# Performance work log

Measured on AMD Instinct MI355X. Metric: run time of the kernel, lower is better.

The kernel has to match this reference:

```python
import jax, jax.numpy as jnp
import numpy as np

N_NODES = 30000
N_EDGES = 480000
NODE_DIM = 16
NUM_RADIAL = 8
NUM_ELEMENTS = 120
R_MAX = 5.0
NUM_BLOCKS = 2
N_PATHS = 5  # h0*sh0->0e, h0*sh1->1o, h0*sh2->2e, h1.sh1->0e, h2.sh2->0e


def _sh_basis(u):
    # real spherical harmonics up to l=2, component normalization, on unit vectors u [E,3]
    x, y, z = u[:, 0], u[:, 1], u[:, 2]
    s15 = jnp.sqrt(jnp.asarray(15.0, u.dtype))
    s5 = jnp.sqrt(jnp.asarray(5.0, u.dtype))
    sh1 = jnp.sqrt(jnp.asarray(3.0, u.dtype)) * u                      # [E,3]
    sh2 = jnp.stack([s15 * x * y, s15 * y * z,
                     0.5 * s5 * (3.0 * z * z - 1.0),
                     s15 * x * z, 0.5 * s15 * (x * x - y * y)], -1)    # [E,5]
    return sh1, sh2


def _energy(pos, emb, W_init, Wr, br, W_out, W_read, W1, b1, W2, b2, z, edge_index):
    N = pos.shape[0]
    row, col = edge_index[0], edge_index[1]
    edge_vec = pos[row] - pos[col]                                     # [E,3] gather
    r = jnp.sqrt(jnp.sum(edge_vec * edge_vec, -1) + 1e-12)             # [E]
    n = jnp.arange(1, NUM_RADIAL + 1, dtype=pos.dtype)
    # Bessel radial basis: sqrt(2/rc) * sin(n*pi*r/rc)/r
    radial = jnp.sqrt(2.0 / R_MAX) * jnp.sin(n[None, :] * jnp.pi * r[:, None] / R_MAX) / r[:, None]  # [E,R]
    u = edge_vec / r[:, None]
    sh1, sh2 = _sh_basis(u)

    # initial projection: embedding scalars -> 0e channels; l=1,l=2 start at zero
    h0 = emb[z] @ W_init                                               # [N,C]
    h1 = jnp.zeros((N, NODE_DIM, 3), pos.dtype)
    h2 = jnp.zeros((N, NODE_DIM, 5), pos.dtype)

    for b in range(NUM_BLOCKS):
        w = (radial @ Wr[b] + br[b]).reshape(-1, N_PATHS, NODE_DIM)    # [E,P,C] radial path weights
        h0c, h1c, h2c = h0[col], h1[col], h2[col]
        # scalar messages: h0*sh0 + <h1,sh1> + <h2,sh2>
        m0 = (w[:, 0] * h0c
              + w[:, 3] * jnp.einsum('ecm,em->ec', h1c, sh1)
              + w[:, 4] * jnp.einsum('ecm,em->ec', h2c, sh2))          # [E,C]
        m1 = (w[:, 1] * h0c)[:, :, None] * sh1[:, None, :]             # [E,C,3]
        m2 = (w[:, 2] * h0c)[:, :, None] * sh2[:, None, :]             # [E,C,5]
        a0 = jax.ops.segment_sum(m0, row, num_segments=N)
        a1 = jax.ops.segment_sum(m1, row, num_segments=N)
        a2 = jax.ops.segment_sum(m2, row, num_segments=N)
        h0 = h0 + a0 @ W_out[b, 0]
        h1 = h1 + jnp.einsum('ncm,cd->ndm', a1, W_out[b, 1])
        h2 = h2 + jnp.einsum('ncm,cd->ndm', a2, W_out[b, 2])

    inv = h0 @ W_read                                                  # readout 0e part
    site = jax.nn.silu(inv @ W1 + b1) @ W2 + b2                        # [N,1]
    return jnp.sum(site)


def setup_inputs() -> dict:
    key = jax.random.key(0)
    ks = jax.random.split(key, 12)
    C, R = NODE_DIM, NUM_RADIAL
    s = 1.0 / np.sqrt(C)
    return {
        'pos': jax.random.normal(ks[0], (N_NODES, 3), jnp.float32) * 3.0,
        'z': jax.random.randint(ks[1], (N_NODES,), 0, NUM_ELEMENTS),
        'edge_index': jax.random.randint(ks[2], (2, N_EDGES), 0, N_NODES),
        'emb': jax.random.normal(ks[3], (NUM_ELEMENTS, C), jnp.float32),
        'W_init': jax.random.normal(ks[4], (C, C), jnp.float32) * s,
        'Wr': jax.random.normal(ks[5], (NUM_BLOCKS, R, N_PATHS * C), jnp.float32) / np.sqrt(R),
        'br': jnp.zeros((NUM_BLOCKS, N_PATHS * C), jnp.float32),
        'W_out': jax.random.normal(ks[6], (NUM_BLOCKS, 3, C, C), jnp.float32) * s,
        'W_read': jax.random.normal(ks[7], (C, C), jnp.float32) * s,
        'W1': jax.random.normal(ks[8], (C, C), jnp.float32) * s,
        'b1': jnp.zeros((C,), jnp.float32),
        'W2': jax.random.normal(ks[9], (C, 1), jnp.float32) * s,
        'b2': jnp.zeros((1,), jnp.float32),
    }


def reference(pos, z, edge_index, emb, W_init, Wr, br, W_out, W_read, W1, b1, W2, b2):
    e_fn = lambda p: _energy(p, emb, W_init, Wr, br, W_out, W_read, W1, b1, W2, b2, z, edge_index)
    total, dE_dpos = jax.value_and_grad(e_fn)(pos)
    energy = jnp.reshape(total, (1, 1))
    forces = -dE_dpos
    return energy, forces
```

## Files before the change

### kernel.cpp

```cpp
#include <hip/hip_runtime.h>
#include <math.h>

#ifndef M_PI
#define M_PI 3.14159265358979323846
#endif

static inline int cdiv(int a, int b){ return (a + b - 1) / b; }

#define SQRT3f  1.7320508075688772f
#define SQRT5f  2.23606797749979f
#define SQRT15f 3.872983346207417f
#define KRADf   0.6324555320336759f
#define PI5f    0.6283185307179586f

__device__ __forceinline__ float grp16_sum(float v){
  v += __shfl_xor(v, 1, 64);
  v += __shfl_xor(v, 2, 64);
  v += __shfl_xor(v, 4, 64);
  v += __shfl_xor(v, 8, 64);
  return v;
}
__device__ __forceinline__ float xgrp_sum(float v){
  v += __shfl_xor(v, 16, 64);
  v += __shfl_xor(v, 32, 64);
  return v;
}

__device__ __forceinline__ void sh_from_u(float ux, float uy, float uz,
                                          float* sh1, float* sh2)
{
  sh1[0] = SQRT3f*ux; sh1[1] = SQRT3f*uy; sh1[2] = SQRT3f*uz;
  sh2[0] = SQRT15f*ux*uy;
  sh2[1] = SQRT15f*uy*uz;
  sh2[2] = 0.5f*SQRT5f*(3.f*uz*uz - 1.f);
  sh2[3] = SQRT15f*ux*uz;
  sh2[4] = 0.5f*SQRT15f*(ux*ux - uy*uy);
}

__device__ __forceinline__ void rad_from_sc(float s1, float c1, float inv_r, float* rad)
{
  float tc = 2.f * c1;
  float sprev = 0.f, s = s1;
  float Ki = KRADf * inv_r;
  #pragma unroll
  for (int k = 0; k < 8; k++) {
    rad[k] = Ki * s;
    float sn = tc*s - sprev; sprev = s; s = sn;
  }
}
__device__ __forceinline__ void rad_drad_from_sc(float s1, float c1, float inv_r,
                                                 float* rad, float* draddr)
{
  float tc = 2.f * c1;
  float sprev = 0.f, s = s1, cprev = 1.f, cc = c1;
  float Ki = KRADf * inv_r;
  const float KPI5 = KRADf * PI5f;
  #pragma unroll
  for (int k = 0; k < 8; k++) {
    rad[k] = Ki * s;
    draddr[k] = (KPI5 * (float)(k+1) * cc - rad[k]) * inv_r;
    float sn = tc*s - sprev; sprev = s; s = sn;
    float cn = tc*cc - cprev; cprev = cc; cc = cn;
  }
}

__global__ void k_hist(const int* __restrict__ ei, int E,
                       int* __restrict__ deg_row, int* __restrict__ deg_col)
{
  int e = blockIdx.x * blockDim.x + threadIdx.x;
  if (e >= E) return;
  atomicAdd(&deg_row[ei[e]], 1);
  atomicAdd(&deg_col[ei[E + e]], 1);
}

__global__ void k_alloc(const int* __restrict__ deg_row, const int* __restrict__ deg_col,
                        int* __restrict__ start_row, int* __restrict__ cur_row,
                        int* __restrict__ start_col, int* __restrict__ cur_col,
                        int* __restrict__ cursors, int N)
{
  int idx = blockIdx.x * blockDim.x + threadIdx.x;
  int lane = threadIdx.x & 63;
  #pragma unroll
  for (int which = 0; which < 2; which++) {
    const int* deg = which ? deg_col : deg_row;
    int* start = which ? start_col : start_row;
    int* cur   = which ? cur_col   : cur_row;
    int v = (idx < N) ? deg[idx] : 0;
    int incl = v;
    #pragma unroll
    for (int d = 1; d < 64; d <<= 1) {
      int y = __shfl_up(incl, d, 64);
      if (lane >= d) incl += y;
    }
    int wtot = __shfl(incl, 63, 64);
    int base = 0;
    if (lane == 63) base = atomicAdd(&cursors[which], wtot);
    base = __shfl(base, 63, 64);
    if (idx < N) { int st = base + incl - v; start[idx] = st; cur[idx] = st; }
  }
}

__global__ void k_scatter_geom(const float* __restrict__ pos, const int* __restrict__ ei, int E,
                               int* __restrict__ cur_row, int* __restrict__ cur_col,
                               float4* __restrict__ uR, float2* __restrict__ scR,
                               float4* __restrict__ uC, float2* __restrict__ scC,
                               int* __restrict__ colR, int* __restrict__ cposR,
                               int* __restrict__ rowC, int* __restrict__ rposC)
{
  int e = blockIdx.x * blockDim.x + threadIdx.x;
  if (e >= E) return;
  int row = ei[e], col = ei[E + e];
  int pr = atomicAdd(&cur_row[row], 1);
  int pc = atomicAdd(&cur_col[col], 1);
  colR[pr] = col; cposR[pr] = pc;
  rowC[pc] = row; rposC[pc] = pr;

  float px = pos[row*3+0] - pos[col*3+0];
  float py = pos[row*3+1] - pos[col*3+1];
  float pz = pos[row*3+2] - pos[col*3+2];
  float r2 = px*px + py*py + pz*pz + 1e-12f;
  float r = sqrtf(r2);
  float inv_r = 1.0f / r;
  float ux = px*inv_r, uy = py*inv_r, uz = pz*inv_r;
  float s1, c1;
  sincosf(r * PI5f, &s1, &c1);
  float4 u4 = make_float4(ux, uy, uz, inv_r);
  float2 sc = make_float2(s1, c1);
  uR[pr] = u4; scR[pr] = sc;
  uC[pc] = u4; scC[pc] = sc;
}

__global__ void k_node_init(const float* __restrict__ emb, const int* __restrict__ z,
                            const float* __restrict__ W_init, float* __restrict__ h0, int N)
{
  __shared__ float sW[256];
  if (threadIdx.x < 256) sW[threadIdx.x] = W_init[threadIdx.x];
  __syncthreads();
  int n = blockIdx.x * blockDim.x + threadIdx.x;
  if (n >= N) return;
  const float* e = emb + z[n]*16;
  float ev[16];
  #pragma unroll
  for (int k = 0; k < 16; k++) ev[k] = e[k];
  #pragma unroll
  for (int c = 0; c < 16; c++) {
    float s = 0.f;
    #pragma unroll
    for (int k = 0; k < 16; k++) s += ev[k] * sW[k*16+c];
    h0[n*16+c] = s;
  }
}

__global__ void k_fwd_b0(const float* __restrict__ Wr, const float* __restrict__ br,
                         const float* __restrict__ h0_in,
                         const float4* __restrict__ uR, const float2* __restrict__ scR,
                         const int* __restrict__ colR,
                         const int* __restrict__ start_row, const int* __restrict__ deg_row,
                         float* __restrict__ a0, float* __restrict__ a1, float* __restrict__ a2,
                         int N)
{
  int n = (blockIdx.x * blockDim.x + threadIdx.x) >> 6;
  int lane = threadIdx.x & 63;
  int g = lane >> 4, c = lane & 15;
  if (n >= N) return;
  float wr0[8], wr1[8], wr2[8];
  #pragma unroll
  for (int k = 0; k < 8; k++) {
    wr0[k] = Wr[k*80 + c];
    wr1[k] = Wr[k*80 + 16 + c];
    wr2[k] = Wr[k*80 + 32 + c];
  }
  float b0v = br[c], b1v = br[16 + c], b2v = br[32 + c];

  float acc0 = 0.f, acc1[3] = {0.f,0.f,0.f}, acc2[5] = {0.f,0.f,0.f,0.f,0.f};

  int i0 = start_row[n] + g, i1 = start_row[n] + deg_row[n];
  float4 Un = {0,0,0,0}; float2 SCn = {0,0};
  float h0n = 0.f;
  if (i0 < i1) {
    Un = uR[i0]; SCn = scR[i0];
    h0n = h0_in[colR[i0]*16 + c];
  }
  for (int i = i0; i < i1; i += 4) {
    float4 U = Un; float2 SC = SCn;
    float h0c = h0n;
    if (i+4 < i1) {
      Un = uR[i+4]; SCn = scR[i+4];
      h0n = h0_in[colR[i+4]*16 + c];
    }
    float rad[8];
    rad_from_sc(SC.x, SC.y, U.w, rad);
    float sh1[3], sh2[5];
    sh_from_u(U.x, U.y, U.z, sh1, sh2);
    float w0 = b0v, w1 = b1v, w2 = b2v;
    #pragma unroll
    for (int k = 0; k < 8; k++) {
      w0 += rad[k]*wr0[k]; w1 += rad[k]*wr1[k]; w2 += rad[k]*wr2[k];
    }
    acc0 += w0*h0c;
    float wh1 = w1*h0c, wh2 = w2*h0c;
    #pragma unroll
    for (int m = 0; m < 3; m++) acc1[m] += wh1*sh1[m];
    #pragma unroll
    for (int m = 0; m < 5; m++) acc2[m] += wh2*sh2[m];
  }
  acc0 = xgrp_sum(acc0);
  #pragma unroll
  for (int m = 0; m < 3; m++) acc1[m] = xgrp_sum(acc1[m]);
  #pragma unroll
  for (int m = 0; m < 5; m++) acc2[m] = xgrp_sum(acc2[m]);
  if (g == 0) {
    a0[n*16 + c] = acc0;
    #pragma unroll
    for (int m = 0; m < 3; m++) a1[n*48 + c*3 + m] = acc1[m];
    #pragma unroll
    for (int m = 0; m < 5; m++) a2[n*80 + c*5 + m] = acc2[m];
  }
}

__global__ void k_fwd_b1(const float* __restrict__ Wr, const float* __restrict__ br,
                         const float* __restrict__ h0_in, const float* __restrict__ h1_in,
                         const float* __restrict__ h2_in,
                         const float4* __restrict__ uR, const float2* __restrict__ scR,
                         const int* __restrict__ colR,
                         const int* __restrict__ start_row, const int* __restrict__ deg_row,
                         float* __restrict__ a0, int N)
{
  int n = (blockIdx.x * blockDim.x + threadIdx.x) >> 6;
  int lane = threadIdx.x & 63;
  int g = lane >> 4, c = lane & 15;
  if (n >= N) return;
  float wr0[8], wr3[8], wr4[8];
  #pragma unroll
  for (int k = 0; k < 8; k++) {
    wr0[k] = Wr[k*80 + c];
    wr3[k] = Wr[k*80 + 48 + c];
    wr4[k] = Wr[k*80 + 64 + c];
  }
  float b0v = br[c], b3v = br[48 + c], b4v = br[64 + c];

  float acc0 = 0.f;
  int i0 = start_row[n] + g, i1 = start_row[n] + deg_row[n];
  float4 Un = {0,0,0,0}; float2 SCn = {0,0};
  float h0n = 0.f, h1n[3] = {0,0,0}, h2n[5] = {0,0,0,0,0};
  if (i0 < i1) {
    int col = colR[i0];
    Un = uR[i0]; SCn = scR[i0];
    h0n = h0_in[col*16 + c];
    #pragma unroll
    for (int m = 0; m < 3; m++) h1n[m] = h1_in[col*48 + c*3 + m];
    #pragma unroll
    for (int m = 0; m < 5; m++) h2n[m] = h2_in[col*80 + c*5 + m];
  }
  for (int i = i0; i < i1; i += 4) {
    float4 U = Un; float2 SC = SCn;
    float h0c = h0n;
    float h1c[3], h2c[5];
    #pragma unroll
    for (int m = 0; m < 3; m++) h1c[m] = h1n[m];
    #pragma unroll
    for (int m = 0; m < 5; m++) h2c[m] = h2n[m];
    if (i+4 < i1) {
      int col = colR[i+4];
      Un = uR[i+4]; SCn = scR[i+4];
      h0n = h0_in[col*16 + c];
      #pragma unroll
      for (int m = 0; m < 3; m++) h1n[m] = h1_in[col*48 + c*3 + m];
      #pragma unroll
      for (int m = 0; m < 5; m++) h2n[m] = h2_in[col*80 + c*5 + m];
    }
    float rad[8];
    rad_from_sc(SC.x, SC.y, U.w, rad);
    float sh1[3], sh2[5];
    sh_from_u(U.x, U.y, U.z, sh1, sh2);
    float w0 = b0v, w3 = b3v, w4 = b4v;
    #pragma unroll
    for (int k = 0; k < 8; k++) {
      w0 += rad[k]*wr0[k]; w3 += rad[k]*wr3[k]; w4 += rad[k]*wr4[k];
    }
    float S1 = 0.f, S2 = 0.f;
    #pragma unroll
    for (int m = 0; m < 3; m++) S1 += h1c[m]*sh1[m];
    #pragma unroll
    for (int m = 0; m < 5; m++) S2 += h2c[m]*sh2[m];
    acc0 += w0*h0c + w3*S1 + w4*S2;
  }
  acc0 = xgrp_sum(acc0);
  if (g == 0) a0[n*16 + c] = acc0;
}

__global__ void k_node_update(const float* __restrict__ h0_in,
                              const float* __restrict__ a0, const float* __restrict__ a1,
                              const float* __restrict__ a2,
                              const float* __restrict__ U,
                              float* __restrict__ h0_out, float* __restrict__ h1_out,
                              float* __restrict__ h2_out, int N)
{
  int idx = blockIdx.x * blockDim.x + threadIdx.x;
  int n = idx >> 4, d = idx & 15;
  if (n >= N) return;
  const float* U0 = U;
  const float* U1 = U + 256;
  const float* U2 = U + 512;
  float s = h0_in[n*16 + d];
  #pragma unroll
  for (int c = 0; c < 16; c++) s += a0[n*16 + c] * U0[c*16 + d];
  h0_out[n*16 + d] = s;
  float v1[3] = {0.f, 0.f, 0.f};
  #pragma unroll
  for (int c = 0; c < 16; c++) {
    float u = U1[c*16 + d];
    #pragma unroll
    for (int m = 0; m < 3; m++) v1[m] += a1[n*48 + c*3 + m] * u;
  }
  #pragma unroll
  for (int m = 0; m < 3; m++) h1_out[n*48 + d*3 + m] = v1[m];
  float v2[5] = {0.f, 0.f, 0.f, 0.f, 0.f};
  #pragma unroll
  for (int c = 0; c < 16; c++) {
    float u = U2[c*16 + d];
    #pragma unroll
    for (int m = 0; m < 5; m++) v2[m] += a2[n*80 + c*5 + m] * u;
  }
  #pragma unroll
  for (int m = 0; m < 5; m++) h2_out[n*80 + d*5 + m] = v2[m];
}

__global__ void __launch_bounds__(256, 1)
k_readout_bwd(const float* __restrict__ h0s1, const float* __restrict__ a0in,
              const float* __restrict__ W_read,
              const float* __restrict__ W1, const float* __restrict__ b1,
              const float* __restrict__ W2, const float* __restrict__ b2,
              const float* __restrict__ U0b1,
              float* __restrict__ g0, float* __restrict__ ga0,
              float* __restrict__ partials, int N)
{
  __shared__ float sWr[256], sW1[256], sU[256], sb1[16], sW2[16], sb2;
  __shared__ float swave[4];
  {
    int t = threadIdx.x;
    if (t < 256) { sWr[t] = W_read[t]; sW1[t] = W1[t]; sU[t] = U0b1[t]; }
// ... 74 lines not shown
  #pragma unroll
  for (int off = 32; off; off >>= 1) s += __shfl_down(s, off, 64);
  __shared__ float sw[2];
  if ((t & 63) == 0) sw[t >> 6] = s;
  __syncthreads();
  if (t == 0) energy[0] = sw[0] + sw[1];
}

__global__ void k_ga(const float* __restrict__ g0, const float* __restrict__ g1,
                     const float* __restrict__ g2, const float* __restrict__ U,
                     float* __restrict__ ga0, float* __restrict__ ga1, float* __restrict__ ga2,
                     int N)
{
  int idx = blockIdx.x * blockDim.x + threadIdx.x;
  int n = idx >> 4, c = idx & 15;
  if (n >= N) return;
  const float* U0 = U;
  const float* U1 = U + 256;
  const float* U2 = U + 512;
  float s = 0.f;
  #pragma unroll
  for (int d = 0; d < 16; d++) s += g0[n*16 + d] * U0[c*16 + d];
  ga0[n*16 + c] = s;
  float v1[3] = {0.f, 0.f, 0.f};
  #pragma unroll
  for (int d = 0; d < 16; d++) {
    float u = U1[c*16 + d];
    #pragma unroll
    for (int m = 0; m < 3; m++) v1[m] += g1[n*48 + d*3 + m] * u;
  }
  #pragma unroll
  for (int m = 0; m < 3; m++) ga1[n*48 + c*3 + m] = v1[m];
  float v2[5] = {0.f, 0.f, 0.f, 0.f, 0.f};
  #pragma unroll
  for (int d = 0; d < 16; d++) {
    float u = U2[c*16 + d];
    #pragma unroll
    for (int m = 0; m < 5; m++) v2[m] += g2[n*80 + d*5 + m] * u;
  }
  #pragma unroll
  for (int m = 0; m < 5; m++) ga2[n*80 + c*5 + m] = v2[m];
}

__global__ void k_bwd_b1_col(const float* __restrict__ Wr, const float* __restrict__ br,
                             const float* __restrict__ h0_in, const float* __restrict__ h1_in,
                             const float* __restrict__ h2_in,
                             const float* __restrict__ ga0,
                             const float4* __restrict__ uC, const float2* __restrict__ scC,
                             const int* __restrict__ rowC,
                             const int* __restrict__ start_col, const int* __restrict__ deg_col,
                             float* __restrict__ g0, float* __restrict__ g1, float* __restrict__ g2,
                             float* __restrict__ dv_col, int N)
{
  int n = (blockIdx.x * blockDim.x + threadIdx.x) >> 6;
  int lane = threadIdx.x & 63;
  int g = lane >> 4, c = lane & 15;
  if (n >= N) return;
  float wr0[8], wr3[8], wr4[8];
  #pragma unroll
  for (int k = 0; k < 8; k++) {
    wr0[k] = Wr[k*80 + c];
    wr3[k] = Wr[k*80 + 48 + c];
    wr4[k] = Wr[k*80 + 64 + c];
  }
  float b0v = br[c], b3v = br[48 + c], b4v = br[64 + c];

  float h0c = h0_in[n*16 + c];
  float h1c[3], h2c[5];
  #pragma unroll
  for (int m = 0; m < 3; m++) h1c[m] = h1_in[n*48 + c*3 + m];
  #pragma unroll
  for (int m = 0; m < 5; m++) h2c[m] = h2_in[n*80 + c*5 + m];

  float accg0 = 0.f, accg1[3] = {0.f,0.f,0.f}, accg2[5] = {0.f,0.f,0.f,0.f,0.f};

  int i0 = start_col[n] + g, i1 = start_col[n] + deg_col[n];
  float4 Un = {0,0,0,0}; float2 SCn = {0,0};
  float dm0n = 0.f;
  if (i0 < i1) {
    Un = uC[i0]; SCn = scC[i0];
    dm0n = ga0[rowC[i0]*16 + c];
  }
  for (int i = i0; i < i1; i += 4) {
    float4 U = Un; float2 SC = SCn;
    float dm0 = dm0n;
    if (i+4 < i1) {
      Un = uC[i+4]; SCn = scC[i+4];
      dm0n = ga0[rowC[i+4]*16 + c];
    }
    float rad[8], draddr[8];
    rad_drad_from_sc(SC.x, SC.y, U.w, rad, draddr);
    float ux = U.x, uy = U.y, uz = U.z, inv_r = U.w;
    float sh1[3], sh2[5];
    sh_from_u(ux, uy, uz, sh1, sh2);

    float w0 = b0v, w3 = b3v, w4 = b4v;
    #pragma unroll
    for (int k = 0; k < 8; k++) {
      w0 += rad[k]*wr0[k]; w3 += rad[k]*wr3[k]; w4 += rad[k]*wr4[k];
    }

    float S1 = 0.f, S2 = 0.f;
    #pragma unroll
    for (int m = 0; m < 3; m++) S1 += h1c[m]*sh1[m];
    #pragma unroll
    for (int m = 0; m < 5; m++) S2 += h2c[m]*sh2[m];

    float dw0 = dm0 * h0c;
    float dw3 = dm0 * S1;
    float dw4 = dm0 * S2;
    float t3 = dm0 * w3, t4 = dm0 * w4;

    accg0 += dm0 * w0;
    #pragma unroll
    for (int m = 0; m < 3; m++) accg1[m] += t3 * sh1[m];
    #pragma unroll
    for (int m = 0; m < 5; m++) accg2[m] += t4 * sh2[m];

    float q1x = t3*h1c[0], q1y = t3*h1c[1], q1z = t3*h1c[2];
    float q0 = t4*h2c[0], q1 = t4*h2c[1], q2 = t4*h2c[2], q3 = t4*h2c[3], q4 = t4*h2c[4];
    float gr = 0.f;
    #pragma unroll
    for (int k = 0; k < 8; k++)
      gr += (dw0*wr0[k] + dw3*wr3[k] + dw4*wr4[k]) * draddr[k];
    float gux = SQRT3f*q1x + SQRT15f*(uy*q0 + uz*q3 + ux*q4);
    float guy = SQRT3f*q1y + SQRT15f*(ux*q0 + uz*q1 - uy*q4);
    float guz = SQRT3f*q1z + SQRT15f*uy*q1 + 3.f*SQRT5f*uz*q2 + SQRT15f*ux*q3;

    gr  = grp16_sum(gr);
    gux = grp16_sum(gux);
    guy = grp16_sum(guy);
    guz = grp16_sum(guz);

    if (c == 0) {
      float gdotu = gux*ux + guy*uy + guz*uz;
      dv_col[i*3+0] = gr*ux + (gux - gdotu*ux)*inv_r;
      dv_col[i*3+1] = gr*uy + (guy - gdotu*uy)*inv_r;
      dv_col[i*3+2] = gr*uz + (guz - gdotu*uz)*inv_r;
    }
  }
  accg0 = xgrp_sum(accg0);
  #pragma unroll
  for (int m = 0; m < 3; m++) accg1[m] = xgrp_sum(accg1[m]);
  #pragma unroll
  for (int m = 0; m < 5; m++) accg2[m] = xgrp_sum(accg2[m]);
  if (g == 0) {
    g0[n*16 + c] += accg0;
    #pragma unroll
    for (int m = 0; m < 3; m++) g1[n*48 + c*3 + m] = accg1[m];
    #pragma unroll
    for (int m = 0; m < 5; m++) g2[n*80 + c*5 + m] = accg2[m];
  }
}

__global__ void k_bwd_b0_row(const float* __restrict__ Wr, const float* __restrict__ br,
                             const float* __restrict__ h0_in,
                             const float* __restrict__ ga0, const float* __restrict__ ga1,
                             const float* __restrict__ ga2,
                             const float4* __restrict__ uR, const float2* __restrict__ scR,
                             const int* __restrict__ colR,
                             const int* __restrict__ start_row, const int* __restrict__ deg_row,
                             float* __restrict__ dv_row, int N)
{
  int n = (blockIdx.x * blockDim.x + threadIdx.x) >> 6;
  int lane = threadIdx.x & 63;
  int g = lane >> 4, c = lane & 15;
  if (n >= N) return;
  float wr0[8], wr1[8], wr2[8];
  #pragma unroll
  for (int k = 0; k < 8; k++) {
    wr0[k] = Wr[k*80 + c];
    wr1[k] = Wr[k*80 + 16 + c];
    wr2[k] = Wr[k*80 + 32 + c];
  }
  float b1v = br[16 + c], b2v = br[32 + c];

  float dm0 = ga0[n*16 + c];
  float dm1[3], dm2[5];
  #pragma unroll
  for (int m = 0; m < 3; m++) dm1[m] = ga1[n*48 + c*3 + m];
  #pragma unroll
  for (int m = 0; m < 5; m++) dm2[m] = ga2[n*80 + c*5 + m];

  int i0 = start_row[n] + g, i1 = start_row[n] + deg_row[n];
  float4 Un = {0,0,0,0}; float2 SCn = {0,0};
  float h0n = 0.f;
  if (i0 < i1) {
    Un = uR[i0]; SCn = scR[i0];
    h0n = h0_in[colR[i0]*16 + c];
  }
  for (int i = i0; i < i1; i += 4) {
    float4 U = Un; float2 SC = SCn;
    float h0c = h0n;
    if (i+4 < i1) {
      Un = uR[i+4]; SCn = scR[i+4];
      h0n = h0_in[colR[i+4]*16 + c];
    }
    float rad[8], draddr[8];
    rad_drad_from_sc(SC.x, SC.y, U.w, rad, draddr);
    float ux = U.x, uy = U.y, uz = U.z, inv_r = U.w;
    float sh1[3], sh2[5];
    sh_from_u(ux, uy, uz, sh1, sh2);

    float w1 = b1v, w2v = b2v;
    #pragma unroll
    for (int k = 0; k < 8; k++) { w1 += rad[k]*wr1[k]; w2v += rad[k]*wr2[k]; }

    float T1 = 0.f, T2 = 0.f;
    #pragma unroll
    for (int m = 0; m < 3; m++) T1 += dm1[m]*sh1[m];
    #pragma unroll
    for (int m = 0; m < 5; m++) T2 += dm2[m]*sh2[m];

    float dw0 = dm0 * h0c;
    float dw1 = h0c * T1;
    float dw2 = h0c * T2;

    float w1h = w1*h0c, w2h = w2v*h0c;
    float q1x = dm1[0]*w1h, q1y = dm1[1]*w1h, q1z = dm1[2]*w1h;
    float q0 = dm2[0]*w2h, q1 = dm2[1]*w2h, q2 = dm2[2]*w2h, q3 = dm2[3]*w2h, q4 = dm2[4]*w2h;

    float gr = 0.f;
    #pragma unroll
    for (int k = 0; k < 8; k++)
      gr += (dw0*wr0[k] + dw1*wr1[k] + dw2*wr2[k]) * draddr[k];
    float gux = SQRT3f*q1x + SQRT15f*(uy*q0 + uz*q3 + ux*q4);
    float guy = SQRT3f*q1y + SQRT15f*(ux*q0 + uz*q1 - uy*q4);
    float guz = SQRT3f*q1z + SQRT15f*uy*q1 + 3.f*SQRT5f*uz*q2 + SQRT15f*ux*q3;

    gr  = grp16_sum(gr);
    gux = grp16_sum(gux);
    guy = grp16_sum(guy);
    guz = grp16_sum(guz);

    if (c == 0) {
      float gdotu = gux*ux + guy*uy + guz*uz;
      dv_row[i*3+0] = gr*ux + (gux - gdotu*ux)*inv_r;
      dv_row[i*3+1] = gr*uy + (guy - gdotu*uy)*inv_r;
      dv_row[i*3+2] = gr*uz + (guz - gdotu*uz)*inv_r;
    }
  }
}

__global__ void k_force(const int* __restrict__ start_row, const int* __restrict__ deg_row,
                        const int* __restrict__ cposR,
                        const int* __restrict__ start_col, const int* __restrict__ deg_col,
                        const int* __restrict__ rposC,
                        const float* __restrict__ dv_col, const float* __restrict__ dv_row,
                        float* __restrict__ force, int N)
{
  int n = blockIdx.x * blockDim.x + threadIdx.x;
  if (n >= N) return;
  float fx = 0.f, fy = 0.f, fz = 0.f;
  int c0 = start_col[n], c1 = c0 + deg_col[n];
  for (int i = c0; i < c1; i++) {
    int rp = rposC[i];
    fx += dv_col[i*3+0] + dv_row[rp*3+0];
    fy += dv_col[i*3+1] + dv_row[rp*3+1];
    fz += dv_col[i*3+2] + dv_row[rp*3+2];
  }
  int r0 = start_row[n], r1 = r0 + deg_row[n];
  for (int i = r0; i < r1; i++) {
    int cp = cposR[i];
    fx -= dv_row[i*3+0] + dv_col[cp*3+0];
    fy -= dv_row[i*3+1] + dv_col[cp*3+1];
    fz -= dv_row[i*3+2] + dv_col[cp*3+2];
  }
  force[n*3+0] = fx; force[n*3+1] = fy; force[n*3+2] = fz;
}

extern "C" void kernel_launch(void* const* d_in, const int* in_sizes, int n_in,
                              void* d_out, int out_size, void* d_ws, size_t ws_size,
                              hipStream_t stream)
{
  const float* pos    = (const float*)d_in[0];
  const int*   z      = (const int*)  d_in[1];
  const int*   ei     = (const int*)  d_in[2];
  const float* emb    = (const float*)d_in[3];
  const float* W_init = (const float*)d_in[4];
  const float* Wr     = (const float*)d_in[5];
  const float* br     = (const float*)d_in[6];
  const float* W_out  = (const float*)d_in[7];
  const float* W_read = (const float*)d_in[8];
  const float* W1     = (const float*)d_in[9];
  const float* b1     = (const float*)d_in[10];
  const float* W2     = (const float*)d_in[11];
  const float* b2     = (const float*)d_in[12];

  const int N = in_sizes[0] / 3;
  const int E = in_sizes[2] / 2;

  const int BLK = 256;
  const int NPB = BLK / 64;
  const int NB_READOUT = cdiv(N, BLK);

  float* f = (float*)d_ws;
  float4* uR  = (float4*)f; f += (size_t)E*4;
  float4* uC  = (float4*)f; f += (size_t)E*4;
  float2* scR = (float2*)f; f += (size_t)E*2;
  float2* scC = (float2*)f; f += (size_t)E*2;
  float* h0_s0 = f; f += (size_t)N*16;
  float* h0_s1 = f; f += (size_t)N*16;
  float* h1_s1 = f; f += (size_t)N*48;
  float* h2_s1 = f; f += (size_t)N*80;
  float* a0    = f; f += (size_t)N*16;
  float* a1    = f; f += (size_t)N*48;
  float* a2    = f; f += (size_t)N*80;
  float* ga0b1 = f; f += (size_t)N*16;
  float* g0    = f; f += (size_t)N*16;
  float* g1    = f; f += (size_t)N*48;
  float* g2    = f; f += (size_t)N*80;
  float* dv_c  = f; f += (size_t)E*3;
  float* dv_r  = f; f += (size_t)E*3;
  float* partials = f; f += (size_t)NB_READOUT;
  int* ip = (int*)f;
  int* cursors   = ip; ip += 2;
  int* deg_row   = ip; ip += N;
  int* deg_col   = ip; ip += N;
  int* start_row = ip; ip += N;
  int* start_col = ip; ip += N;
  int* cur_row   = ip; ip += N;
  int* cur_col   = ip; ip += N;
  int* colR      = ip; ip += E;
  int* cposR     = ip; ip += E;
  int* rowC      = ip; ip += E;
  int* rposC     = ip; ip += E;

  float* out    = (float*)d_out;
  float* energy = out;
  float* force  = out + 1;

  (void)hipMemsetAsync(cursors, 0, (size_t)(2 + 2*N) * sizeof(int), stream);

  k_hist<<<cdiv(E, BLK), BLK, 0, stream>>>(ei, E, deg_row, deg_col);
  k_alloc<<<cdiv(N, BLK), BLK, 0, stream>>>(deg_row, deg_col, start_row, cur_row,
                                            start_col, cur_col, cursors, N);
  k_scatter_geom<<<cdiv(E, BLK), BLK, 0, stream>>>(pos, ei, E, cur_row, cur_col,
                                                   uR, scR, uC, scC,
                                                   colR, cposR, rowC, rposC);

  k_node_init<<<cdiv(N, BLK), BLK, 0, stream>>>(emb, z, W_init, h0_s0, N);

  k_fwd_b0<<<cdiv(N, NPB), BLK, 0, stream>>>(Wr, br, h0_s0, uR, scR, colR,
                                             start_row, deg_row, a0, a1, a2, N);
  k_node_update<<<cdiv(N*16, BLK), BLK, 0, stream>>>(h0_s0, a0, a1, a2,
                                                     W_out, h0_s1, h1_s1, h2_s1, N);

  k_fwd_b1<<<cdiv(N, NPB), BLK, 0, stream>>>(Wr + 640, br + 80,
                                             h0_s1, h1_s1, h2_s1, uR, scR, colR,
                                             start_row, deg_row, a0, N);

  k_readout_bwd<<<NB_READOUT, BLK, 0, stream>>>(h0_s1, a0, W_read, W1, b1, W2, b2,
                                                W_out + 768, g0, ga0b1, partials, N);
  k_energy<<<1, 128, 0, stream>>>(partials, NB_READOUT, energy);

  k_bwd_b1_col<<<cdiv(N, NPB), BLK, 0, stream>>>(Wr + 640, br + 80,
                                                 h0_s1, h1_s1, h2_s1, ga0b1,
                                                 uC, scC, rowC, start_col, deg_col,
                                                 g0, g1, g2, dv_c, N);

  k_ga<<<cdiv(N*16, BLK), BLK, 0, stream>>>(g0, g1, g2, W_out, a0, a1, a2, N);
  k_bwd_b0_row<<<cdiv(N, NPB), BLK, 0, stream>>>(Wr, br, h0_s0,
                                                 a0, a1, a2, uR, scR, colR,
                                                 start_row, deg_row, dv_r, N);

  k_force<<<cdiv(N, BLK), BLK, 0, stream>>>(start_row, deg_row, cposR,
                                            start_col, deg_col, rposC,
                                            dv_c, dv_r, force, N);
}
```

Before: 497.3 us.

## Use persistent grid-stride edge kernels, fuse radial recurrence, parallelize force gather

The four per-node edge kernels now run as persistent grid-stride loops with a fixed grid of 2048 blocks. This amortizes the per-warp loading of the radial weight registers across many nodes. The radial basis and its derivative are computed inline within the weight accumulation, and the derivative dot product is folded into two scalar accumulators, which avoids holding rad/draddr arrays and lowers register pressure. The force kernel uses 16 lanes per node with a shuffle reduction instead of one thread walking all edges. The fixed grid size may limit load balance or occupancy on skewed degree distributions.

New measurement: 473.4 us. 4.8% less time.

```diff
diff --git a/kernel.cpp b/kernel.cpp
--- a/kernel.cpp
+++ b/kernel.cpp
@@ -12,6 +12,8 @@
 #define SQRT15f 3.872983346207417f
 #define KRADf   0.6324555320336759f
 #define PI5f    0.6283185307179586f
+#define KPI5f   (KRADf * PI5f)
+
 
 __device__ __forceinline__ float grp16_sum(float v){
   v += __shfl_xor(v, 1, 64);
@@ -37,32 +39,6 @@
   sh2[4] = 0.5f*SQRT15f*(ux*ux - uy*uy);
 }
 
-__device__ __forceinline__ void rad_from_sc(float s1, float c1, float inv_r, float* rad)
-{
-  float tc = 2.f * c1;
-  float sprev = 0.f, s = s1;
-  float Ki = KRADf * inv_r;
-  #pragma unroll
-  for (int k = 0; k < 8; k++) {
-    rad[k] = Ki * s;
-    float sn = tc*s - sprev; sprev = s; s = sn;
-  }
-}
-__device__ __forceinline__ void rad_drad_from_sc(float s1, float c1, float inv_r,
-                                                 float* rad, float* draddr)
-{
-  float tc = 2.f * c1;
-  float sprev = 0.f, s = s1, cprev = 1.f, cc = c1;
-  float Ki = KRADf * inv_r;
-  const float KPI5 = KRADf * PI5f;
-  #pragma unroll
-  for (int k = 0; k < 8; k++) {
-    rad[k] = Ki * s;
-    draddr[k] = (KPI5 * (float)(k+1) * cc - rad[k]) * inv_r;
-    float sn = tc*s - sprev; sprev = s; s = sn;
-    float cn = tc*cc - cprev; cprev = cc; cc = cn;
-  }
-}
 
 __global__ void k_hist(const int* __restrict__ ei, int E,
                        int* __restrict__ deg_row, int* __restrict__ deg_col)
@@ -159,10 +135,10 @@
                          float* __restrict__ a0, float* __restrict__ a1, float* __restrict__ a2,
                          int N)
 {
-  int n = (blockIdx.x * blockDim.x + threadIdx.x) >> 6;
+  int wid = (blockIdx.x * blockDim.x + threadIdx.x) >> 6;
+  int nw  = (gridDim.x * blockDim.x) >> 6;
   int lane = threadIdx.x & 63;
   int g = lane >> 4, c = lane & 15;
-  if (n >= N) return;
   float wr0[8], wr1[8], wr2[8];
   #pragma unroll
   for (int k = 0; k < 8; k++) {
@@ -172,49 +148,54 @@
   }
   float b0v = br[c], b1v = br[16 + c], b2v = br[32 + c];
 
-  float acc0 = 0.f, acc1[3] = {0.f,0.f,0.f}, acc2[5] = {0.f,0.f,0.f,0.f,0.f};
-
-  int i0 = start_row[n] + g, i1 = start_row[n] + deg_row[n];
-  float4 Un = {0,0,0,0}; float2 SCn = {0,0};
-  float h0n = 0.f;
-  if (i0 < i1) {
-    Un = uR[i0]; SCn = scR[i0];
-    h0n = h0_in[colR[i0]*16 + c];
-  }
-  for (int i = i0; i < i1; i += 4) {
-    float4 U = Un; float2 SC = SCn;
-    float h0c = h0n;
-    if (i+4 < i1) {
-      Un = uR[i+4]; SCn = scR[i+4];
-      h0n = h0_in[colR[i+4]*16 + c];
-    }
-    float rad[8];
-    rad_from_sc(SC.x, SC.y, U.w, rad);
-    float sh1[3], sh2[5];
-    sh_from_u(U.x, U.y, U.z, sh1, sh2);
-    float w0 = b0v, w1 = b1v, w2 = b2v;
-    #pragma unroll
-    for (int k = 0; k < 8; k++) {
-      w0 += rad[k]*wr0[k]; w1 += rad[k]*wr1[k]; w2 += rad[k]*wr2[k];
-    }
-    acc0 += w0*h0c;
-    float wh1 = w1*h0c, wh2 = w2*h0c;
-    #pragma unroll
-    for (int m = 0; m < 3; m++) acc1[m] += wh1*sh1[m];
-    #pragma unroll
-    for (int m = 0; m < 5; m++) acc2[m] += wh2*sh2[m];
-  }
-  acc0 = xgrp_sum(acc0);
-  #pragma unroll
-  for (int m = 0; m < 3; m++) acc1[m] = xgrp_sum(acc1[m]);
-  #pragma unroll
-  for (int m = 0; m < 5; m++) acc2[m] = xgrp_sum(acc2[m]);
-  if (g == 0) {
-    a0[n*16 + c] = acc0;
-    #pragma unroll
-    for (int m = 0; m < 3; m++) a1[n*48 + c*3 + m] = acc1[m];
-    #pragma unroll
-    for (int m = 0; m < 5; m++) a2[n*80 + c*5 + m] = acc2[m];
+  for (int n = wid; n < N; n += nw) {
+    float acc0 = 0.f, acc1[3] = {0.f,0.f,0.f}, acc2[5] = {0.f,0.f,0.f,0.f,0.f};
+
+    int i0 = start_row[n] + g, i1 = start_row[n] + deg_row[n];
+    float4 Un = {0,0,0,0}; float2 SCn = {0,0};
+    float h0n = 0.f;
+    if (i0 < i1) {
+      Un = uR[i0]; SCn = scR[i0];
+      h0n = h0_in[colR[i0]*16 + c];
+    }
+    for (int i = i0; i < i1; i += 4) {
+      float4 U = Un; float2 SC = SCn;
+      float h0c = h0n;
+      if (i+4 < i1) {
+        Un = uR[i+4]; SCn = scR[i+4];
+        h0n = h0_in[colR[i+4]*16 + c];
+      }
+      float Ki = KRADf * U.w;
+      float tc = 2.f * SC.y;
+      float sprev = 0.f, s = SC.x;
+      float w0 = b0v, w1 = b1v, w2 = b2v;
+      #pragma unroll
+      for (int k = 0; k < 8; k++) {
+        float rad = Ki * s;
+        w0 += rad*wr0[k]; w1 += rad*wr1[k]; w2 += rad*wr2[k];
+        float sn = tc*s - sprev; sprev = s; s = sn;
+      }
+      float sh1[3], sh2[5];
+      sh_from_u(U.x, U.y, U.z, sh1, sh2);
+      acc0 += w0*h0c;
+      float wh1 = w1*h0c, wh2 = w2*h0c;
+      #pragma unroll
+      for (int m = 0; m < 3; m++) acc1[m] += wh1*sh1[m];
+      #pragma unroll
+      for (int m = 0; m < 5; m++) acc2[m] += wh2*sh2[m];
+    }
+    acc0 = xgrp_sum(acc0);
+    #pragma unroll
+    for (int m = 0; m < 3; m++) acc1[m] = xgrp_sum(acc1[m]);
+    #pragma unroll
+    for (int m = 0; m < 5; m++) acc2[m] = xgrp_sum(acc2[m]);
+    if (g == 0) {
+      a0[n*16 + c] = acc0;
+      #pragma unroll
+      for (int m = 0; m < 3; m++) a1[n*48 + c*3 + m] = acc1[m];
+      #pragma unroll
+      for (int m = 0; m < 5; m++) a2[n*80 + c*5 + m] = acc2[m];
+    }
   }
 }
 
@@ -226,10 +207,10 @@
                          const int* __restrict__ start_row, const int* __restrict__ deg_row,
                          float* __restrict__ a0, int N)
 {
-  int n = (blockIdx.x * blockDim.x + threadIdx.x) >> 6;
+  int wid = (blockIdx.x * blockDim.x + threadIdx.x) >> 6;
+  int nw  = (gridDim.x * blockDim.x) >> 6;
   int lane = threadIdx.x & 63;
   int g = lane >> 4, c = lane & 15;
-  if (n >= N) return;
   float wr0[8], wr3[8], wr4[8];
   #pragma unroll
   for (int k = 0; k < 8; k++) {
@@ -239,54 +220,59 @@
   }
   float b0v = br[c], b3v = br[48 + c], b4v = br[64 + c];
 
-  float acc0 = 0.f;
-  int i0 = start_row[n] + g, i1 = start_row[n] + deg_row[n];
-  float4 Un = {0,0,0,0}; float2 SCn = {0,0};
-  float h0n = 0.f, h1n[3] = {0,0,0}, h2n[5] = {0,0,0,0,0};
-  if (i0 < i1) {
-    int col = colR[i0];
-    Un = uR[i0]; SCn = scR[i0];
-    h0n = h0_in[col*16 + c];
-    #pragma unroll
-    for (int m = 0; m < 3; m++) h1n[m] = h1_in[col*48 + c*3 + m];
-    #pragma unroll
-    for (int m = 0; m < 5; m++) h2n[m] = h2_in[col*80 + c*5 + m];
-  }
-  for (int i = i0; i < i1; i += 4) {
-    float4 U = Un; float2 SC = SCn;
-    float h0c = h0n;
-    float h1c[3], h2c[5];
-    #pragma unroll
-    for (int m = 0; m < 3; m++) h1c[m] = h1n[m];
-    #pragma unroll
-    for (int m = 0; m < 5; m++) h2c[m] = h2n[m];
-    if (i+4 < i1) {
-      int col = colR[i+4];
-      Un = uR[i+4]; SCn = scR[i+4];
+  for (int n = wid; n < N; n += nw) {
+    float acc0 = 0.f;
+    int i0 = start_row[n] + g, i1 = start_row[n] + deg_row[n];
+    float4 Un = {0,0,0,0}; float2 SCn = {0,0};
+    float h0n = 0.f, h1n[3] = {0,0,0}, h2n[5] = {0,0,0,0,0};
+    if (i0 < i1) {
+      int col = colR[i0];
+      Un = uR[i0]; SCn = scR[i0];
       h0n = h0_in[col*16 + c];
       #pragma unroll
       for (int m = 0; m < 3; m++) h1n[m] = h1_in[col*48 + c*3 + m];
       #pragma unroll
       for (int m = 0; m < 5; m++) h2n[m] = h2_in[col*80 + c*5 + m];
     }
-    float rad[8];
-    rad_from_sc(SC.x, SC.y, U.w, rad);
-    float sh1[3], sh2[5];
-    sh_from_u(U.x, U.y, U.z, sh1, sh2);
-    float w0 = b0v, w3 = b3v, w4 = b4v;
-    #pragma unroll
-    for (int k = 0; k < 8; k++) {
-      w0 += rad[k]*wr0[k]; w3 += rad[k]*wr3[k]; w4 += rad[k]*wr4[k];
-    }
-    float S1 = 0.f, S2 = 0.f;
-    #pragma unroll
-    for (int m = 0; m < 3; m++) S1 += h1c[m]*sh1[m];
-    #pragma unroll
-    for (int m = 0; m < 5; m++) S2 += h2c[m]*sh2[m];
-    acc0 += w0*h0c + w3*S1 + w4*S2;
-  }
-  acc0 = xgrp_sum(acc0);
-  if (g == 0) a0[n*16 + c] = acc0;
+    for (int i = i0; i < i1; i += 4) {
+      float4 U = Un; float2 SC = SCn;
+      float h0c = h0n;
+      float h1c[3], h2c[5];
+      #pragma unroll
+      for (int m = 0; m < 3; m++) h1c[m] = h1n[m];
+      #pragma unroll
+      for (int m = 0; m < 5; m++) h2c[m] = h2n[m];
+      if (i+4 < i1) {
+        int col = colR[i+4];
+        Un = uR[i+4]; SCn = scR[i+4];
+        h0n = h0_in[col*16 + c];
+        #pragma unroll
+        for (int m = 0; m < 3; m++) h1n[m] = h1_in[col*48 + c*3 + m];
+        #pragma unroll
+        for (int m = 0; m < 5; m++) h2n[m] = h2_in[col*80 + c*5 + m];
+      }
+      float Ki = KRADf * U.w;
+      float tc = 2.f * SC.y;
+      float sprev = 0.f, s = SC.x;
+      float w0 = b0v, w3 = b3v, w4 = b4v;
+      #pragma unroll
+      for (int k = 0; k < 8; k++) {
+        float rad = Ki * s;
+        w0 += rad*wr0[k]; w3 += rad*wr3[k]; w4 += rad*wr4[k];
+        float sn = tc*s - sprev; sprev = s; s = sn;
+      }
+      float sh1[3], sh2[5];
+      sh_from_u(U.x, U.y, U.z, sh1, sh2);
+      float S1 = 0.f, S2 = 0.f;
+      #pragma unroll
+      for (int m = 0; m < 3; m++) S1 += h1c[m]*sh1[m];
+      #pragma unroll
+      for (int m = 0; m < 5; m++) S2 += h2c[m]*sh2[m];
+      acc0 += w0*h0c + w3*S1 + w4*S2;
+    }
+    acc0 = xgrp_sum(acc0);
+    if (g == 0) a0[n*16 + c] = acc0;
+  }
 }
 
 __global__ void k_node_update(const float* __restrict__ h0_in,
@@ -467,10 +453,10 @@
                              float* __restrict__ g0, float* __restrict__ g1, float* __restrict__ g2,
                              float* __restrict__ dv_col, int N)
 {
-  int n = (blockIdx.x * blockDim.x + threadIdx.x) >> 6;
+  int wid = (blockIdx.x * blockDim.x + threadIdx.x) >> 6;
+  int nw  = (gridDim.x * blockDim.x) >> 6;
   int lane = threadIdx.x & 63;
   int g = lane >> 4, c = lane & 15;
-  if (n >= N) return;
   float wr0[8], wr3[8], wr4[8];
   #pragma unroll
   for (int k = 0; k < 8; k++) {
@@ -480,91 +466,98 @@
   }
   float b0v = br[c], b3v = br[48 + c], b4v = br[64 + c];
 
-  float h0c = h0_in[n*16 + c];
-  float h1c[3], h2c[5];
-  #pragma unroll
-  for (int m = 0; m < 3; m++) h1c[m] = h1_in[n*48 + c*3 + m];
-  #pragma unroll
-  for (int m = 0; m < 5; m++) h2c[m] = h2_in[n*80 + c*5 + m];
-
-  float accg0 = 0.f, accg1[3] = {0.f,0.f,0.f}, accg2[5] = {0.f,0.f,0.f,0.f,0.f};
-
-  int i0 = start_col[n] + g, i1 = start_col[n] + deg_col[n];
-  float4 Un = {0,0,0,0}; float2 SCn = {0,0};
-  float dm0n = 0.f;
-  if (i0 < i1) {
-    Un = uC[i0]; SCn = scC[i0];
-    dm0n = ga0[rowC[i0]*16 + c];
-  }
-  for (int i = i0; i < i1; i += 4) {
-    float4 U = Un; float2 SC = SCn;
-    float dm0 = dm0n;
-    if (i+4 < i1) {
-      Un = uC[i+4]; SCn = scC[i+4];
-      dm0n = ga0[rowC[i+4]*16 + c];
-    }
-    float rad[8], draddr[8];
-    rad_drad_from_sc(SC.x, SC.y, U.w, rad, draddr);
-    float ux = U.x, uy = U.y, uz = U.z, inv_r = U.w;
-    float sh1[3], sh2[5];
-    sh_from_u(ux, uy, uz, sh1, sh2);
-
-    float w0 = b0v, w3 = b3v, w4 = b4v;
-    #pragma unroll
-    for (int k = 0; k < 8; k++) {
-      w0 += rad[k]*wr0[k]; w3 += rad[k]*wr3[k]; w4 += rad[k]*wr4[k];
-    }
-
-    float S1 = 0.f, S2 = 0.f;
-    #pragma unroll
-    for (int m = 0; m < 3; m++) S1 += h1c[m]*sh1[m];
-    #pragma unroll
-    for (int m = 0; m < 5; m++) S2 += h2c[m]*sh2[m];
-
-    float dw0 = dm0 * h0c;
-    float dw3 = dm0 * S1;
-    float dw4 = dm0 * S2;
-    float t3 = dm0 * w3, t4 = dm0 * w4;
-
-    accg0 += dm0 * w0;
-    #pragma unroll
-    for (int m = 0; m < 3; m++) accg1[m] += t3 * sh1[m];
-    #pragma unroll
-    for (int m = 0; m < 5; m++) accg2[m] += t4 * sh2[m];
-
-    float q1x = t3*h1c[0], q1y = t3*h1c[1], q1z = t3*h1c[2];
-    float q0 = t4*h2c[0], q1 = t4*h2c[1], q2 = t4*h2c[2], q3 = t4*h2c[3], q4 = t4*h2c[4];
-    float gr = 0.f;
-    #pragma unroll
-    for (int k = 0; k < 8; k++)
-      gr += (dw0*wr0[k] + dw3*wr3[k] + dw4*wr4[k]) * draddr[k];
-    float gux = SQRT3f*q1x + SQRT15f*(uy*q0 + uz*q3 + ux*q4);
-    float guy = SQRT3f*q1y + SQRT15f*(ux*q0 + uz*q1 - uy*q4);
-    float guz = SQRT3f*q1z + SQRT15f*uy*q1 + 3.f*SQRT5f*uz*q2 + SQRT15f*ux*q3;
-
-    gr  = grp16_sum(gr);
-    gux = grp16_sum(gux);
-    guy = grp16_sum(guy);
-    guz = grp16_sum(guz);
-
-    if (c == 0) {
-      float gdotu = gux*ux + guy*uy + guz*uz;
-      dv_col[i*3+0] = gr*ux + (gux - gdotu*ux)*inv_r;
-      dv_col[i*3+1] = gr*uy + (guy - gdotu*uy)*inv_r;
-      dv_col[i*3+2] = gr*uz + (guz - gdotu*uz)*inv_r;
-    }
-  }
-  accg0 = xgrp_sum(accg0);
-  #pragma unroll
-  for (int m = 0; m < 3; m++) accg1[m] = xgrp_sum(accg1[m]);
-  #pragma unroll
-  for (int m = 0; m < 5; m++) accg2[m] = xgrp_sum(accg2[m]);
-  if (g == 0) {
-    g0[n*16 + c] += accg0;
-    #pragma unroll
-    for (int m = 0; m < 3; m++) g1[n*48 + c*3 + m] = accg1[m];
-    #pragma unroll
-    for (int m = 0; m < 5; m++) g2[n*80 + c*5 + m] = accg2[m];
+  for (int n = wid; n < N; n += nw) {
+    float h0c = h0_in[n*16 + c];
+    float h1c[3], h2c[5];
+    #pragma unroll
+    for (int m = 0; m < 3; m++) h1c[m] = h1_in[n*48 + c*3 + m];
+    #pragma unroll
+    for (int m = 0; m < 5; m++) h2c[m] = h2_in[n*80 + c*5 + m];
+
+    float accg0 = 0.f, accg1[3] = {0.f,0.f,0.f}, accg2[5] = {0.f,0.f,0.f,0.f,0.f};
+
+    int i0 = start_col[n] + g, i1 = start_col[n] + deg_col[n];
+    float4 Un = {0,0,0,0}; float2 SCn = {0,0};
+    float dm0n = 0.f;
+    if (i0 < i1) {
+      Un = uC[i0]; SCn = scC[i0];
+      dm0n = ga0[rowC[i0]*16 + c];
+    }
+    for (int i = i0; i < i1; i += 4) {
+      float4 U = Un; float2 SC = SCn;
+      float dm0 = dm0n;
+      if (i+4 < i1) {
+        Un = uC[i+4]; SCn = scC[i+4];
+        dm0n = ga0[rowC[i+4]*16 + c];
+      }
+      float ux = U.x, uy = U.y, uz = U.z, inv_r = U.w;
+      float sh1[3], sh2[5];
+      sh_from_u(ux, uy, uz, sh1, sh2);
+
+      float S1 = 0.f, S2 = 0.f;
+      #pragma unroll
+      for (int m = 0; m < 3; m++) S1 += h1c[m]*sh1[m];
+      #pragma unroll
+      for (int m = 0; m < 5; m++) S2 += h2c[m]*sh2[m];
+
+      float dw0 = dm0 * h0c;
+      float dw3 = dm0 * S1;
+      float dw4 = dm0 * S2;
+
+      float Ki = KRADf * inv_r;
+      float tc = 2.f * SC.y;
+      float sprev = 0.f, s = SC.x, cprev = 1.f, cc = SC.y;
+      float w0 = b0v, w3 = b3v, w4 = b4v;
+      float P = 0.f, Q = 0.f;
+      #pragma unroll
+      for (int k = 0; k < 8; k++) {
+        float rad = Ki * s;
+        w0 += rad*wr0[k]; w3 += rad*wr3[k]; w4 += rad*wr4[k];
+        float t = dw0*wr0[k] + dw3*wr3[k] + dw4*wr4[k];
+        P = fmaf(t*cc, (float)(k+1), P);
+        Q = fmaf(t, rad, Q);
+        float sn = tc*s - sprev; sprev = s; s = sn;
+        float cn = tc*cc - cprev; cprev = cc; cc = cn;
+      }
+
+      float t3 = dm0 * w3, t4 = dm0 * w4;
+      accg0 += dm0 * w0;
+      #pragma unroll
+      for (int m = 0; m < 3; m++) accg1[m] += t3 * sh1[m];
+      #pragma unroll
+      for (int m = 0; m < 5; m++) accg2[m] += t4 * sh2[m];
+
+      float q1x = t3*h1c[0], q1y = t3*h1c[1], q1z = t3*h1c[2];
+      float q0 = t4*h2c[0], q1 = t4*h2c[1], q2 = t4*h2c[2], q3 = t4*h2c[3], q4 = t4*h2c[4];
+      float gr = (KPI5f*P - Q) * inv_r;
+      float gux = SQRT3f*q1x + SQRT15f*(uy*q0 + uz*q3 + ux*q4);
+      float guy = SQRT3f*q1y + SQRT15f*(ux*q0 + uz*q1 - uy*q4);
+      float guz = SQRT3f*q1z + SQRT15f*uy*q1 + 3.f*SQRT5f*uz*q2 + SQRT15f*ux*q3;
+
+      gr  = grp16_sum(gr);
+      gux = grp16_sum(gux);
+      guy = grp16_sum(guy);
+      guz = grp16_sum(guz);
+
+      if (c == 0) {
+        float gdotu = gux*ux + guy*uy + guz*uz;
+        dv_col[i*3+0] = gr*ux + (gux - gdotu*ux)*inv_r;
+        dv_col[i*3+1] = gr*uy + (guy - gdotu*uy)*inv_r;
+        dv_col[i*3+2] = gr*uz + (guz - gdotu*uz)*inv_r;
+      }
+    }
+    accg0 = xgrp_sum(accg0);
+    #pragma unroll
+    for (int m = 0; m < 3; m++) accg1[m] = xgrp_sum(accg1[m]);
+    #pragma unroll
+    for (int m = 0; m < 5; m++) accg2[m] = xgrp_sum(accg2[m]);
+    if (g == 0) {
+      g0[n*16 + c] += accg0;
+      #pragma unroll
+      for (int m = 0; m < 3; m++) g1[n*48 + c*3 + m] = accg1[m];
+      #pragma unroll
+      for (int m = 0; m < 5; m++) g2[n*80 + c*5 + m] = accg2[m];
+    }
   }
 }
 
@@ -577,10 +570,10 @@
                              const int* __restrict__ start_row, const int* __restrict__ deg_row,
                              float* __restrict__ dv_row, int N)
 {
-  int n = (blockIdx.x * blockDim.x + threadIdx.x) >> 6;
+  int wid = (blockIdx.x * blockDim.x + threadIdx.x) >> 6;
+  int nw  = (gridDim.x * blockDim.x) >> 6;
   int lane = threadIdx.x & 63;
   int g = lane >> 4, c = lane & 15;
-  if (n >= N) return;
   float wr0[8], wr1[8], wr2[8];
   #pragma unroll
   for (int k = 0; k < 8; k++) {
@@ -590,69 +583,78 @@
   }
   float b1v = br[16 + c], b2v = br[32 + c];
 
-  float dm0 = ga0[n*16 + c];
-  float dm1[3], dm2[5];
-  #pragma unroll
-  for (int m = 0; m < 3; m++) dm1[m] = ga1[n*48 + c*3 + m];
-  #pragma unroll
-  for (int m = 0; m < 5; m++) dm2[m] = ga2[n*80 + c*5 + m];
-
-  int i0 = start_row[n] + g, i1 = start_row[n] + deg_row[n];
-  float4 Un = {0,0,0,0}; float2 SCn = {0,0};
-  float h0n = 0.f;
-  if (i0 < i1) {
-    Un = uR[i0]; SCn = scR[i0];
-    h0n = h0_in[colR[i0]*16 + c];
-  }
-  for (int i = i0; i < i1; i += 4) {
-    float4 U = Un; float2 SC = SCn;
-    float h0c = h0n;
-    if (i+4 < i1) {
-      Un = uR[i+4]; SCn = scR[i+4];
-      h0n = h0_in[colR[i+4]*16 + c];
-    }
-    float rad[8], draddr[8];
-    rad_drad_from_sc(SC.x, SC.y, U.w, rad, draddr);
-    float ux = U.x, uy = U.y, uz = U.z, inv_r = U.w;
-    float sh1[3], sh2[5];
-    sh_from_u(ux, uy, uz, sh1, sh2);
-
-    float w1 = b1v, w2v = b2v;
-    #pragma unroll
-    for (int k = 0; k < 8; k++) { w1 += rad[k]*wr1[k]; w2v += rad[k]*wr2[k]; }
-
-    float T1 = 0.f, T2 = 0.f;
-    #pragma unroll
-    for (int m = 0; m < 3; m++) T1 += dm1[m]*sh1[m];
-    #pragma unroll
-    for (int m = 0; m < 5; m++) T2 += dm2[m]*sh2[m];
-
-    float dw0 = dm0 * h0c;
-    float dw1 = h0c * T1;
-    float dw2 = h0c * T2;
-
-    float w1h = w1*h0c, w2h = w2v*h0c;
-    float q1x = dm1[0]*w1h, q1y = dm1[1]*w1h, q1z = dm1[2]*w1h;
-    float q0 = dm2[0]*w2h, q1 = dm2[1]*w2h, q2 = dm2[2]*w2h, q3 = dm2[3]*w2h, q4 = dm2[4]*w2h;
-
-    float gr = 0.f;
-    #pragma unroll
-    for (int k = 0; k < 8; k++)
-      gr += (dw0*wr0[k] + dw1*wr1[k] + dw2*wr2[k]) * draddr[k];
-    float gux = SQRT3f*q1x + SQRT15f*(uy*q0 + uz*q3 + ux*q4);
-    float guy = SQRT3f*q1y + SQRT15f*(ux*q0 + uz*q1 - uy*q4);
-    float guz = SQRT3f*q1z + SQRT15f*uy*q1 + 3.f*SQRT5f*uz*q2 + SQRT15f*ux*q3;
-
-    gr  = grp16_sum(gr);
-    gux = grp16_sum(gux);
-    guy = grp16_sum(guy);
-    guz = grp16_sum(guz);
-
-    if (c == 0) {
-      float gdotu = gux*ux + guy*uy + guz*uz;
-      dv_row[i*3+0] = gr*ux + (gux - gdotu*ux)*inv_r;
-      dv_row[i*3+1] = gr*uy + (guy - gdotu*uy)*inv_r;
-      dv_row[i*3+2] = gr*uz + (guz - gdotu*uz)*inv_r;
+  for (int n = wid; n < N; n += nw) {
+    float dm0 = ga0[n*16 + c];
+    float dm1[3], dm2[5];
+    #pragma unroll
+    for (int m = 0; m < 3; m++) dm1[m] = ga1[n*48 + c*3 + m];
+    #pragma unroll
+    for (int m = 0; m < 5; m++) dm2[m] = ga2[n*80 + c*5 + m];
+
+    int i0 = start_row[n] + g, i1 = start_row[n] + deg_row[n];
+    float4 Un = {0,0,0,0}; float2 SCn = {0,0};
+    float h0n = 0.f;
+    if (i0 < i1) {
+      Un = uR[i0]; SCn = scR[i0];
+      h0n = h0_in[colR[i0]*16 + c];
+    }
+    for (int i = i0; i < i1; i += 4) {
+      float4 U = Un; float2 SC = SCn;
+      float h0c = h0n;
+      if (i+4 < i1) {
+        Un = uR[i+4]; SCn = scR[i+4];
+        h0n = h0_in[colR[i+4]*16 + c];
+      }
+      float ux = U.x, uy = U.y, uz = U.z, inv_r = U.w;
+      float sh1[3], sh2[5];
+      sh_from_u(ux, uy, uz, sh1, sh2);
+
+      float T1 = 0.f, T2 = 0.f;
+      #pragma unroll
+      for (int m = 0; m < 3; m++) T1 += dm1[m]*sh1[m];
+      #pragma unroll
+      for (int m = 0; m < 5; m++) T2 += dm2[m]*sh2[m];
+
+      float dw0 = dm0 * h0c;
+      float dw1 = h0c * T1;
+      float dw2 = h0c * T2;
+
+      float Ki = KRADf * inv_r;
+      float tc = 2.f * SC.y;
+      float sprev = 0.f, s = SC.x, cprev = 1.f, cc = SC.y;
+      float w1 = b1v, w2v = b2v;
+      float P = 0.f, Q = 0.f;
+      #pragma unroll
+      for (int k = 0; k < 8; k++) {
+        float rad = Ki * s;
+        w1 += rad*wr1[k]; w2v += rad*wr2[k];
+        float t = dw0*wr0[k] + dw1*wr1[k] + dw2*wr2[k];
+        P = fmaf(t*cc, (float)(k+1), P);
+        Q = fmaf(t, rad, Q);
+        float sn = tc*s - sprev; sprev = s; s = sn;
+        float cn = tc*cc - cprev; cprev = cc; cc = cn;
+      }
+
+      float w1h = w1*h0c, w2h = w2v*h0c;
+      float q1x = dm1[0]*w1h, q1y = dm1[1]*w1h, q1z = dm1[2]*w1h;
+      float q0 = dm2[0]*w2h, q1 = dm2[1]*w2h, q2 = dm2[2]*w2h, q3 = dm2[3]*w2h, q4 = dm2[4]*w2h;
+
+      float gr = (KPI5f*P - Q) * inv_r;
+      float gux = SQRT3f*q1x + SQRT15f*(uy*q0 + uz*q3 + ux*q4);
+      float guy = SQRT3f*q1y + SQRT15f*(ux*q0 + uz*q1 - uy*q4);
+      float guz = SQRT3f*q1z + SQRT15f*uy*q1 + 3.f*SQRT5f*uz*q2 + SQRT15f*ux*q3;
+
+      gr  = grp16_sum(gr);
+      gux = grp16_sum(gux);
+      guy = grp16_sum(guy);
+      guz = grp16_sum(guz);
+
+      if (c == 0) {
+        float gdotu = gux*ux + guy*uy + guz*uz;
+        dv_row[i*3+0] = gr*ux + (gux - gdotu*ux)*inv_r;
+        dv_row[i*3+1] = gr*uy + (guy - gdotu*uy)*inv_r;
+        dv_row[i*3+2] = gr*uz + (guz - gdotu*uz)*inv_r;
+      }
     }
   }
 }
@@ -664,24 +666,28 @@
                         const float* __restrict__ dv_col, const float* __restrict__ dv_row,
                         float* __restrict__ force, int N)
 {
-  int n = blockIdx.x * blockDim.x + threadIdx.x;
+  int idx = blockIdx.x * blockDim.x + threadIdx.x;
+  int n = idx >> 4, l = idx & 15;
   if (n >= N) return;
   float fx = 0.f, fy = 0.f, fz = 0.f;
   int c0 = start_col[n], c1 = c0 + deg_col[n];
-  for (int i = c0; i < c1; i++) {
+  for (int i = c0 + l; i < c1; i += 16) {
     int rp = rposC[i];
     fx += dv_col[i*3+0] + dv_row[rp*3+0];
     fy += dv_col[i*3+1] + dv_row[rp*3+1];
     fz += dv_col[i*3+2] + dv_row[rp*3+2];
   }
   int r0 = start_row[n], r1 = r0 + deg_row[n];
-  for (int i = r0; i < r1; i++) {
+  for (int i = r0 + l; i < r1; i += 16) {
     int cp = cposR[i];
     fx -= dv_row[i*3+0] + dv_col[cp*3+0];
     fy -= dv_row[i*3+1] + dv_col[cp*3+1];
     fz -= dv_row[i*3+2] + dv_col[cp*3+2];
   }
-  force[n*3+0] = fx; force[n*3+1] = fy; force[n*3+2] = fz;
+  fx = grp16_sum(fx); fy = grp16_sum(fy); fz = grp16_sum(fz);
+  if (l == 0) {
+    force[n*3+0] = fx; force[n*3+1] = fy; force[n*3+2] = fz;
+  }
 }
 
 extern "C" void kernel_launch(void* const* d_in, const int* in_sizes, int n_in,
@@ -706,8 +712,8 @@
   const int E = in_sizes[2] / 2;
 
   const int BLK = 256;
-  const int NPB = BLK / 64;
   const int NB_READOUT = cdiv(N, BLK);
+  const int PBLK = (N < 8192) ? cdiv(N, 4) : 2048;
 
   float* f = (float*)d_ws;
   float4* uR  = (float4*)f; f += (size_t)E*4;
@@ -756,30 +762,30 @@
 
   k_node_init<<<cdiv(N, BLK), BLK, 0, stream>>>(emb, z, W_init, h0_s0, N);
 
-  k_fwd_b0<<<cdiv(N, NPB), BLK, 0, stream>>>(Wr, br, h0_s0, uR, scR, colR,
-                                             start_row, deg_row, a0, a1, a2, N);
+  k_fwd_b0<<<PBLK, BLK, 0, stream>>>(Wr, br, h0_s0, uR, scR, colR,
+                                     start_row, deg_row, a0, a1, a2, N);
   k_node_update<<<cdiv(N*16, BLK), BLK, 0, stream>>>(h0_s0, a0, a1, a2,
                                                      W_out, h0_s1, h1_s1, h2_s1, N);
 
-  k_fwd_b1<<<cdiv(N, NPB), BLK, 0, stream>>>(Wr + 640, br + 80,
-                                             h0_s1, h1_s1, h2_s1, uR, scR, colR,
-                                             start_row, deg_row, a0, N);
+  k_fwd_b1<<<PBLK, BLK, 0, stream>>>(Wr + 640, br + 80,
+                                     h0_s1, h1_s1, h2_s1, uR, scR, colR,
+                                     start_row, deg_row, a0, N);
 
   k_readout_bwd<<<NB_READOUT, BLK, 0, stream>>>(h0_s1, a0, W_read, W1, b1, W2, b2,
                                                 W_out + 768, g0, ga0b1, partials, N);
   k_energy<<<1, 128, 0, stream>>>(partials, NB_READOUT, energy);
 
-  k_bwd_b1_col<<<cdiv(N, NPB), BLK, 0, stream>>>(Wr + 640, br + 80,
-                                                 h0_s1, h1_s1, h2_s1, ga0b1,
-                                                 uC, scC, rowC, start_col, deg_col,
-                                                 g0, g1, g2, dv_c, N);
+  k_bwd_b1_col<<<PBLK, BLK, 0, stream>>>(Wr + 640, br + 80,
+                                         h0_s1, h1_s1, h2_s1, ga0b1,
+                                         uC, scC, rowC, start_col, deg_col,
+                                         g0, g1, g2, dv_c, N);
 
   k_ga<<<cdiv(N*16, BLK), BLK, 0, stream>>>(g0, g1, g2, W_out, a0, a1, a2, N);
-  k_bwd_b0_row<<<cdiv(N, NPB), BLK, 0, stream>>>(Wr, br, h0_s0,
-                                                 a0, a1, a2, uR, scR, colR,
-                                                 start_row, deg_row, dv_r, N);
-
-  k_force<<<cdiv(N, BLK), BLK, 0, stream>>>(start_row, deg_row, cposR,
-                                            start_col, deg_col, rposC,
-                                            dv_c, dv_r, force, N);
-}
+  k_bwd_b0_row<<<PBLK, BLK, 0, stream>>>(Wr, br, h0_s0,
+                                         a0, a1, a2, uR, scR, colR,
+                                         start_row, deg_row, dv_r, N);
+
+  k_force<<<cdiv(N*16, BLK), BLK, 0, stream>>>(start_row, deg_row, cposR,
+                                               start_col, deg_col, rposC,
+                                               dv_c, dv_r, force, N);
+}
```
